# Performance work log

Hardware: AMD Instinct MI355X
Metric: run time of the kernel (lower is better)

Reference implementation:

```python
import jax, jax.numpy as jnp
import numpy as np
from jax import lax

C = 64
RED = 8
BN_EPS = 1e-5

def _conv1x1(x, W, b):
    # x: [N,C,H,W], W: [O,C] (1x1 conv kernel squeezed), b: [O]
    return jnp.einsum('nchw,oc->nohw', x, W) + b[None, :, None, None]

def _cross_attention(img, depth, Wq, bq, Wk, bk, Wv, bv, gamma):
    # img, depth: [N,C,H,W]; channel-channel attention (attn is [N,C,C])
    N, c, H, Wd = img.shape
    HW = H * Wd
    q = _conv1x1(img, Wq, bq).reshape(N, c, HW).astype(jnp.float32)
    k = _conv1x1(depth, Wk, bk).reshape(N, c, HW).astype(jnp.float32)
    v = _conv1x1(depth, Wv, bv).reshape(N, c, HW).astype(jnp.float32)
    attn = jax.nn.softmax(jnp.einsum('nci,ndi->ncd', q, k), axis=-1)  # [N,C,C]
    out = jnp.einsum('ncd,ndi->nci', attn, v).reshape(N, c, H, Wd).astype(img.dtype)
    return gamma * out + img

def _mlp(x, w1, b1, w2, b2):
    h = jax.nn.relu(x @ w1.T + b1)
    return h @ w2.T + b2

def _cbam(x, fc1_w, fc1_b, fc2_w, fc2_b, sa_w, sa_b):
    # x: [N,C,H,W]
    avg = x.mean(axis=(2, 3))          # [N,C]
    mx = x.max(axis=(2, 3))            # [N,C]
    ch = jax.nn.sigmoid(_mlp(avg, fc1_w, fc1_b, fc2_w, fc2_b)
                        + _mlp(mx, fc1_w, fc1_b, fc2_w, fc2_b))  # [N,C]
    x = x * ch[:, :, None, None]
    sp_in = jnp.stack([x.mean(axis=1), x.max(axis=1)], axis=1)   # [N,2,H,W]
    sp = lax.conv_general_dilated(sp_in, sa_w, (1, 1), 'SAME',
                                  dimension_numbers=('NCHW', 'OIHW', 'NCHW')) + sa_b[None, :, None, None]
    return x * jax.nn.sigmoid(sp)


def setup_inputs() -> dict:
    key = jax.random.key(0)
    ks = jax.random.split(key, 20)
    B, S, H, W = 2, 8, 128, 128
    s = 0.05
    d = {
        'img_feat': jax.random.normal(ks[0], (B, S, C, H, W), jnp.float32),
        'depth_feat': jax.random.normal(ks[1], (B, S, C, H, W), jnp.float32),
        # CrossAttention (shared module, used for both directions)
        'Wq': jax.random.normal(ks[2], (C, C), jnp.float32) * s,
        'bq': jax.random.normal(ks[3], (C,), jnp.float32) * s,
        'Wk': jax.random.normal(ks[4], (C, C), jnp.float32) * s,
        'bk': jax.random.normal(ks[5], (C,), jnp.float32) * s,
        'Wv': jax.random.normal(ks[6], (C, C), jnp.float32) * s,
        'bv': jax.random.normal(ks[7], (C,), jnp.float32) * s,
        'gamma': jax.random.normal(ks[8], (1,), jnp.float32) * 0.5,
        # fusion conv (3x3, 2C -> C) + BN (inference, running stats)
        'Wf': jax.random.normal(ks[9], (C, 2 * C, 3, 3), jnp.float32) * s,
        'bf': jax.random.normal(ks[10], (C,), jnp.float32) * s,
        'bn_g': jnp.ones((C,), jnp.float32),
        'bn_b': jnp.zeros((C,), jnp.float32),
        'bn_m': jax.random.normal(ks[11], (C,), jnp.float32) * s,
        'bn_v': jax.random.uniform(ks[12], (C,), jnp.float32, 0.5, 1.5),
        # CBAM channel MLP + spatial conv (7x7, 2 -> 1)
        'fc1_w': jax.random.normal(ks[13], (C // RED, C), jnp.float32) * s,
        'fc1_b': jax.random.normal(ks[14], (C // RED,), jnp.float32) * s,
        'fc2_w': jax.random.normal(ks[15], (C, C // RED), jnp.float32) * s,
        'fc2_b': jax.random.normal(ks[16], (C,), jnp.float32) * s,
        'sa_w': jax.random.normal(ks[17], (1, 2, 7, 7), jnp.float32) * s,
        'sa_b': jax.random.normal(ks[18], (1,), jnp.float32) * s,
    }
    return d


def reference(img_feat, depth_feat, Wq, bq, Wk, bk, Wv, bv, gamma,
              Wf, bf, bn_g, bn_b, bn_m, bn_v,
              fc1_w, fc1_b, fc2_w, fc2_b, sa_w, sa_b):
    B, S, c, H, W = img_feat.shape
    img = img_feat.reshape(-1, c, H, W)
    dep = depth_feat.reshape(-1, c, H, W)
    img_att = _cross_attention(img, dep, Wq, bq, Wk, bk, Wv, bv, gamma)
    dep_att = _cross_attention(dep, img, Wq, bq, Wk, bk, Wv, bv, gamma)
    fused = jnp.concatenate([img_att, dep_att], axis=1)  # [N,2C,H,W]
    fused = lax.conv_general_dilated(fused, Wf, (1, 1), 'SAME',
                                     dimension_numbers=('NCHW', 'OIHW', 'NCHW')) + bf[None, :, None, None]
    inv = bn_g * lax.rsqrt(bn_v + BN_EPS)
    fused = jax.nn.relu(fused * inv[None, :, None, None] + (bn_b - bn_m * inv)[None, :, None, None])
    fused = _cbam(fused, fc1_w, fc1_b, fc2_w, fc2_b, sa_w, sa_b)
    return fused.reshape(B, S, c, H, W)
```

## Files before the change

### kernel.cpp

```cpp
#include <hip/hip_runtime.h>
#include <math.h>


typedef __bf16 bf16_t;
typedef bf16_t bf16x8 __attribute__((ext_vector_type(8)));
typedef bf16_t bf16x4 __attribute__((ext_vector_type(4)));
typedef float  f32x4  __attribute__((ext_vector_type(4)));
typedef _Float16 f16_t;
typedef f16_t  f16x8  __attribute__((ext_vector_type(8)));

static constexpr int  CH  = 64;
static constexpr int  H   = 128;
static constexpr int  W   = 128;
static constexpr int  HW  = H * W;
static constexpr int  NI  = 16;
static constexpr int  NCK = 16;

static constexpr int W_WQ=0, W_BQ=4096, W_WK=4160, W_BK=8256, W_WV=8320, W_BV=12416,
  W_GAMMA=12480, W_WF=12481, W_BF=86209, W_BNG=86273, W_BNB=86337, W_BNM=86401,
  W_BNV=86465, W_FC1W=86529, W_FC1B=87041, W_FC2W=87049, W_FC2B=87561,
  W_SAW=87625, W_SAB=87723, W_TOTAL=87724;

static constexpr size_t OFF_GPART  = 0;
static constexpr size_t SZ_GPART   = (size_t)NI*NCK*4096*4;
static constexpr size_t OFF_SX     = OFF_GPART + SZ_GPART;
static constexpr size_t SZ_SXY     = (size_t)NI*NCK*64*4;
static constexpr size_t OFF_SY     = OFF_SX + SZ_SXY;
static constexpr size_t OFF_M1     = OFF_SY + SZ_SXY;
static constexpr size_t SZ_M       = (size_t)NI*4096*4;
static constexpr size_t OFF_M2     = OFF_M1 + SZ_M;
static constexpr size_t OFF_T1     = OFF_M2 + SZ_M;
static constexpr size_t SZ_T       = (size_t)NI*64*4;
static constexpr size_t OFF_T2     = OFF_T1 + SZ_T;
static constexpr size_t OFF_BCONST = OFF_T2 + SZ_T;
static constexpr size_t OFF_WH     = OFF_BCONST + 256;
static constexpr size_t SZ_WH      = (size_t)NI*64*9*128*2;
static constexpr size_t OFF_WINDT  = OFF_WH + SZ_WH;
static constexpr size_t SZ_WIND    = (size_t)NI*9*64*4;
static constexpr size_t OFF_IND    = OFF_WINDT + SZ_WIND;
static constexpr size_t OFF_BSUM   = OFF_IND + SZ_WIND;
static constexpr size_t SZ_BST     = (size_t)NI*64*64*4;
static constexpr size_t OFF_BMAX   = OFF_BSUM + SZ_BST;
static constexpr size_t OFF_CHS    = OFF_BMAX + SZ_BST;
static constexpr size_t OFF_SPIN   = OFF_CHS + SZ_T;
static constexpr size_t SZ_SPIN    = (size_t)NI*2*HW*4;
static constexpr size_t OFF_FLAG   = OFF_SPIN + SZ_SPIN;
static constexpr size_t OFF_WF32   = OFF_FLAG + 256;
static constexpr size_t OFF_WFT    = ((OFF_WF32 + (size_t)W_TOTAL*4 + 255) / 256) * 256;
static constexpr size_t SZ_WFT     = (size_t)9*8192*4;
static constexpr size_t OFF_P16    = ((OFF_WFT + SZ_WFT + 255) / 256) * 256;
static constexpr size_t SZ_P16     = (size_t)NI*4*HW*32*2;

__global__ __launch_bounds__(256) void k0_detect(
    const unsigned short* __restrict__ u, int* __restrict__ flag)
{
  __shared__ int bad;
  if (threadIdx.x == 0) bad = 0;
  __syncthreads();
  int local = 0;
  for (int i = threadIdx.x; i < 4096; i += 256) {
    const unsigned short v = u[2*i];
    const int e = (v >> 7) & 0xFF;
    if (e >= 0xC0) local = 1;
  }
  if (local) atomicOr(&bad, 1);
  __syncthreads();
  if (threadIdx.x == 0) flag[0] = bad;
}

struct WPack { const void* p[19]; int sz[19]; int off[19]; };

__global__ __launch_bounds__(256) void kw_convert(
    WPack wp, const int* __restrict__ flag, float* __restrict__ dst,
    float* __restrict__ WFT)
{
  const int j = blockIdx.y;
  const int i = blockIdx.x * 256 + threadIdx.x;
  if (i >= wp.sz[j]) return;
  const int f32m = flag[0];
  float v;
  if (f32m) v = ((const float*)wp.p[j])[i];
  else      v = (float)((const bf16_t*)wp.p[j])[i];
  dst[wp.off[j] + i] = v;
  if (j == 7) WFT[(i % 9) * 8192 + (i / 9)] = v;
}

__global__ __launch_bounds__(256) void kc_pack(
    const bf16_t* __restrict__ Xb, const bf16_t* __restrict__ Yb,
    const float* __restrict__ Xf, const float* __restrict__ Yf,
    const int* __restrict__ flag, f16_t* __restrict__ P16)
{
  const int lin = blockIdx.x * 256 + threadIdx.x;
  const int oct = lin & 3;
  const int p   = (lin >> 2) & 16383;
  const int s   = (lin >> 16) & 3;
  const int n   = lin >> 18;
  const int f32m = flag[0];
  const size_t nbase = (size_t)n * CH * HW;
  const int c0 = (s & 1) * 32 + oct * 8;
  const float*  Fsrc = (s < 2) ? Xf : Yf;
  const bf16_t* Bsrc = (s < 2) ? Xb : Yb;
  f16x8 h;
  #pragma unroll
  for (int j = 0; j < 8; ++j) {
    const size_t q = nbase + (size_t)(c0 + j) * HW + p;
    const float v = f32m ? Fsrc[q] : (float)Bsrc[q];
    h[j] = (f16_t)v;
  }
  *(f16x8*)(P16 + (size_t)lin * 8) = h;
}

__global__ __launch_bounds__(256) void k1_gram(
    const bf16_t* __restrict__ Xb, const bf16_t* __restrict__ Yb,
    const float* __restrict__ Xf, const float* __restrict__ Yf,
    const int* __restrict__ flag,
    float* __restrict__ Gpart, float* __restrict__ sxpart, float* __restrict__ sypart)
{
  const int chunk = blockIdx.x, n = blockIdx.y;
  const int t = threadIdx.x, lane = t & 63, wv = t >> 6;
  const int mrow = lane & 15, quad = lane >> 4;
  const int f32m = flag[0];
  const size_t nbase = (size_t)n * CH * HW;
  const int p0 = chunk * 1024 + wv * 256;

  f32x4 acc[4][4], acc2[4][4];
  #pragma unroll
  for (int i = 0; i < 4; ++i)
    #pragma unroll
    for (int j = 0; j < 4; ++j) {
      acc[i][j]  = (f32x4){0.f, 0.f, 0.f, 0.f};
      acc2[i][j] = (f32x4){0.f, 0.f, 0.f, 0.f};
    }
  float sxl[4] = {0.f,0.f,0.f,0.f}, syl[4] = {0.f,0.f,0.f,0.f};

  for (int kt = 0; kt < 8; ++kt) {
    const int pk = p0 + kt * 32 + quad * 8;
    if (f32m) {
      bf16x8 a[4], b[4], al[4], bl[4];
      #pragma unroll
      for (int mt = 0; mt < 4; ++mt) {
        const size_t ia = nbase + (size_t)(mt*16 + mrow) * HW + pk;
        float sa = 0.f, sb = 0.f;
        #pragma unroll
        for (int j = 0; j < 8; ++j) {
          const float va = Xf[ia + j];
          const bf16_t ha = (bf16_t)va;
          a[mt][j] = ha; al[mt][j] = (bf16_t)(va - (float)ha); sa += va;
          const float vb = Yf[ia + j];
          const bf16_t hb = (bf16_t)vb;
          b[mt][j] = hb; bl[mt][j] = (bf16_t)(vb - (float)hb); sb += vb;
        }
        sxl[mt] += sa; syl[mt] += sb;
      }
      #pragma unroll
      for (int mt = 0; mt < 4; ++mt)
        #pragma unroll
        for (int nt = 0; nt < 4; ++nt) {
          acc[mt][nt]  = __builtin_amdgcn_mfma_f32_16x16x32_bf16(a[mt],  b[nt],  acc[mt][nt],  0, 0, 0);
          acc2[mt][nt] = __builtin_amdgcn_mfma_f32_16x16x32_bf16(a[mt],  bl[nt], acc2[mt][nt], 0, 0, 0);
          acc2[mt][nt] = __builtin_amdgcn_mfma_f32_16x16x32_bf16(al[mt], b[nt],  acc2[mt][nt], 0, 0, 0);
        }
    } else {
      bf16x8 a[4], b[4];
      #pragma unroll
      for (int mt = 0; mt < 4; ++mt) {
        const size_t ia = nbase + (size_t)(mt*16 + mrow) * HW + pk;
        a[mt] = *(const bf16x8*)(Xb + ia);
        b[mt] = *(const bf16x8*)(Yb + ia);
        float sa = 0.f, sb = 0.f;
        #pragma unroll
        for (int j = 0; j < 8; ++j) { sa += (float)a[mt][j]; sb += (float)b[mt][j]; }
        sxl[mt] += sa; syl[mt] += sb;
      }
      #pragma unroll
      for (int mt = 0; mt < 4; ++mt)
        #pragma unroll
        for (int nt = 0; nt < 4; ++nt)
          acc[mt][nt] = __builtin_amdgcn_mfma_f32_16x16x32_bf16(a[mt], b[nt], acc[mt][nt], 0, 0, 0);
    }
  }

  #pragma unroll
  for (int mt = 0; mt < 4; ++mt) {
    sxl[mt] += __shfl_xor(sxl[mt], 16, 64); sxl[mt] += __shfl_xor(sxl[mt], 32, 64);
    syl[mt] += __shfl_xor(syl[mt], 16, 64); syl[mt] += __shfl_xor(syl[mt], 32, 64);
  }

  __shared__ float Gs[4096];
  __shared__ float sxs[64], sys[64];
  for (int w2 = 0; w2 < 4; ++w2) {
    if (wv == w2) {
      #pragma unroll
      for (int mt = 0; mt < 4; ++mt) {
        #pragma unroll
        for (int nt = 0; nt < 4; ++nt) {
          #pragma unroll
          for (int r = 0; r < 4; ++r) {
            const int c = mt*16 + quad*4 + r, d = nt*16 + mrow;
            const float val = acc[mt][nt][r] + acc2[mt][nt][r];
            if (w2 == 0) Gs[c*64 + d]  = val;
            else         Gs[c*64 + d] += val;
          }
        }
        if (quad == 0) {
          const int c = mt*16 + mrow;
          if (w2 == 0) { sxs[c] = sxl[mt];  sys[c] = syl[mt]; }
          else         { sxs[c] += sxl[mt]; sys[c] += syl[mt]; }
        }
      }
    }
    __syncthreads();
  }
  float* Gp = Gpart + ((size_t)n*NCK + chunk) * 4096;
  for (int i = t; i < 4096; i += 256) Gp[i] = Gs[i];
  if (t < 64)       sxpart[((size_t)n*NCK + chunk)*64 + t]        = sxs[t];
  else if (t < 128) sypart[((size_t)n*NCK + chunk)*64 + (t - 64)] = sys[t - 64];
}

__global__ __launch_bounds__(256, 1) void k2a_attn(
    const float* __restrict__ Gpart, const float* __restrict__ sxpart, const float* __restrict__ sypart,
    const float* __restrict__ wt,
    float* __restrict__ M1, float* __restrict__ M2,
    float* __restrict__ T1, float* __restrict__ T2)
{
  const int n = blockIdx.x, t = threadIdx.x;
  constexpr int SW = 68;
  __shared__ float Gs[4096];
  __shared__ float P1s[4096], P2s[4096];
  __shared__ float A1s[64*SW], A2s[64*SW];
  __shared__ float WQs[64*SW], WKs[64*SW], WVs[64*SW];
  __shared__ float sxs[64], sys[64], ux[64], uy[64], vx[64], vy[64];

  for (int i = t; i < 4096; i += 256) {
    const int r = i >> 6, cc = i & 63;
    WQs[r*SW + cc] = wt[W_WQ + i];
    WKs[r*SW + cc] = wt[W_WK + i];
    WVs[r*SW + cc] = wt[W_WV + i];
  }
  for (int i4 = t; i4 < 1024; i4 += 256) {
    f32x4 s = (f32x4){0.f, 0.f, 0.f, 0.f};
    for (int c2 = 0; c2 < NCK; ++c2)
      s += *(const f32x4*)(Gpart + ((size_t)n*NCK + c2)*4096 + i4*4);
    *(f32x4*)(Gs + i4*4) = s;
  }
  if (t < 64) {
    float s = 0.f; for (int c2 = 0; c2 < NCK; ++c2) s += sxpart[((size_t)n*NCK + c2)*64 + t];
    sxs[t] = s;
  } else if (t < 128) {
    const int c = t - 64;
    float s = 0.f; for (int c2 = 0; c2 < NCK; ++c2) s += sypart[((size_t)n*NCK + c2)*64 + c];
    sys[c] = s;
  }
  __syncthreads();

  {
    const int e = t & 63;
    float Greg[64], GTreg[64];
    #pragma unroll
    for (int a = 0; a < 64; ++a) Greg[a] = Gs[a*64 + e];
    #pragma unroll
    for (int a4 = 0; a4 < 16; ++a4)
      *(f32x4*)(GTreg + a4*4) = *(const f32x4*)(Gs + e*64 + a4*4);
    for (int it = 0; it < 16; ++it) {
      const int c = (t >> 6) + 4*it;
      float s1 = 0.f, s2 = 0.f;
      #pragma unroll
      for (int a4 = 0; a4 < 16; ++a4) {
        const f32x4 w4 = *(const f32x4*)(WQs + c*SW + a4*4);
        #pragma unroll
        for (int r = 0; r < 4; ++r) {
          s1 += w4[r] * Greg[a4*4 + r];
          s2 += w4[r] * GTreg[a4*4 + r];
        }
      }
      P1s[c*64 + e] = s1; P2s[c*64 + e] = s2;
    }
  }
  {
    const int which = t >> 6, c = t & 63;
    const float* Wrow = (which < 2) ? (WQs + c*SW) : (WKs + c*SW);
    const float* vecv = ((which & 1) == 0) ? sxs : sys;
    float s = 0.f;
    #pragma unroll
    for (int a = 0; a < 64; ++a) s += Wrow[a] * vecv[a];
    if      (which == 0) ux[c] = s;
    else if (which == 1) uy[c] = s;
    else if (which == 2) vx[c] = s;
    else                 vy[c] = s;
  }
  __syncthreads();

  {
    const int d = t & 63;
    float WKreg[64];
    #pragma unroll
    for (int a4 = 0; a4 < 16; ++a4)
      *(f32x4*)(WKreg + a4*4) = *(const f32x4*)(WKs + d*SW + a4*4);
    const float bkd = wt[W_BK + d];
    for (int it = 0; it < 16; ++it) {
      const int c = (t >> 6) + 4*it;
      float s1 = 0.f, s2 = 0.f;
      #pragma unroll
      for (int e4 = 0; e4 < 16; ++e4) {
        const f32x4 p1 = *(const f32x4*)(P1s + c*64 + e4*4);
        const f32x4 p2 = *(const f32x4*)(P2s + c*64 + e4*4);
        #pragma unroll
        for (int r = 0; r < 4; ++r) {
          s1 += p1[r] * WKreg[e4*4 + r];
          s2 += p2[r] * WKreg[e4*4 + r];
        }
      }
      const float bqc = wt[W_BQ + c];
      s1 += ux[c]*bkd + bqc*vy[d] + 16384.f*bqc*bkd;
      s2 += uy[c]*bkd + bqc*vx[d] + 16384.f*bqc*bkd;
      A1s[c*SW + d] = s1; A2s[c*SW + d] = s2;
    }
  }
  __syncthreads();

  if (t < 128) {
    float* R = (t < 64) ? (A1s + t*SW) : (A2s + (t - 64)*SW);
    float m = R[0];
    for (int d = 1; d < 64; ++d) m = fmaxf(m, R[d]);
    float s = 0.f;
    for (int d = 0; d < 64; ++d) { const float e2 = expf(R[d] - m); R[d] = e2; s += e2; }
    const float inv = 1.f / s;
    for (int d = 0; d < 64; ++d) R[d] *= inv;
  }
  __syncthreads();

  {
    const int e = t & 63;
    float WVreg[64];
    #pragma unroll
    for (int dd = 0; dd < 64; ++dd) WVreg[dd] = WVs[dd*SW + e];
    for (int it = 0; it < 16; ++it) {
      const int c = (t >> 6) + 4*it;
      float s1 = 0.f, s2 = 0.f;
      #pragma unroll
      for (int d4 = 0; d4 < 16; ++d4) {
        const f32x4 a1 = *(const f32x4*)(A1s + c*SW + d4*4);
        const f32x4 a2 = *(const f32x4*)(A2s + c*SW + d4*4);
        #pragma unroll
        for (int r = 0; r < 4; ++r) {
          s1 += a1[r] * WVreg[d4*4 + r];
          s2 += a2[r] * WVreg[d4*4 + r];
        }
      }
      M1[(size_t)n*4096 + c*64 + e] = s1;
      M2[(size_t)n*4096 + c*64 + e] = s2;
    }
  }
  if (t < 64) {
    float s1 = 0.f, s2 = 0.f;
    for (int d = 0; d < 64; ++d) {
      const float b = wt[W_BV + d];
      s1 += A1s[t*SW + d] * b;
      s2 += A2s[t*SW + d] * b;
    }
    T1[n*64 + t] = s1; T2[n*64 + t] = s2;
  }
}

__global__ __launch_bounds__(256) void k2b_weff(
    const float* __restrict__ wt, const float* __restrict__ WFT,
    const float* __restrict__ M1, const float* __restrict__ M2,
    const float* __restrict__ T1, const float* __restrict__ T2,
    f16_t* __restrict__ Wh, float* __restrict__ windT, float* __restrict__ bconst)
{
  const int tap = blockIdx.x, dir = blockIdx.y, n = blockIdx.z;
  const int t = threadIdx.x;
  const float g = wt[W_GAMMA];
  f16_t* Whn = Wh + (size_t)n * 64 * 9 * 128;
  const float* Mo = (dir == 0) ? (M2 + (size_t)n*4096) : (M1 + (size_t)n*4096);

  __shared__ float Wfs[8192];
  __shared__ float Ms[4096];

  for (int i4 = t; i4 < 2048; i4 += 256)
    *(f32x4*)(Wfs + i4*4) = *(const f32x4*)(WFT + (size_t)tap*8192 + i4*4);
  for (int i4 = t; i4 < 1024; i4 += 256)
    *(f32x4*)(Ms + i4*4) = *(const f32x4*)(Mo + i4*4);
  __syncthreads();

  const int e = t & 63;
  float Msreg[64];
  #pragma unroll
  for (int c = 0; c < 64; ++c) Msreg[c] = Ms[c*64 + e];
  const int coff = dir ? 0 : 64;
  const int boff = dir ? 64 : 0;
  for (int it = 0; it < 16; ++it) {
    const int o = (t >> 6) + 4*it;
    const float inv = wt[W_BNG + o] * rsqrtf(wt[W_BNV + o] + 1e-5f);
    const float base = Wfs[o*128 + boff + e];
    float s = 0.f;
    #pragma unroll
    for (int c4 = 0; c4 < 16; ++c4) {
      const f32x4 w4 = *(const f32x4*)(Wfs + o*128 + coff + c4*4);
      #pragma unroll
      for (int r = 0; r < 4; ++r) s += w4[r] * Msreg[c4*4 + r];
    }
    Whn[(o*9 + tap)*128 + dir*64 + e] = (f16_t)(inv * (base + g * s));
  }

  if (dir == 0 && t < 64) {
    const int o = t;
    const float inv = wt[W_BNG + o] * rsqrtf(wt[W_BNV + o] + 1e-5f);
    float s = 0.f;
    for (int c = 0; c < 64; ++c)
      s += wt[W_WF + (o*128 + c)*9 + tap]      * T1[n*64 + c]
         + wt[W_WF + (o*128 + 64 + c)*9 + tap] * T2[n*64 + c];
    windT[((size_t)n*9 + tap)*64 + o] = inv * g * s;
    if (tap == 0 && n == 0)
      bconst[o] = wt[W_BF + o]*inv + wt[W_BNB + o] - wt[W_BNM + o]*inv;
  }
}

__global__ __launch_bounds__(512) void k3_conv(
    const bf16_t* __restrict__ Xb, const bf16_t* __restrict__ Yb,
    const float* __restrict__ Xf, const float* __restrict__ Yf,
    const int* __restrict__ flag,
    const f16_t* __restrict__ Wh, const float* __restrict__ bconst,
    const float* __restrict__ windT,
    const f16_t* __restrict__ P16, const int useP16,
    bf16_t* __restrict__ fusedB, float* __restrict__ fusedF,
    float* __restrict__ bsum, float* __restrict__ bmax)
{
  __shared__ __attribute__((aligned(16))) f16_t sbuf[6][130][40];
  __shared__ float sind[576], sconst[64];
  __shared__ float ssum[8][64], smax[8][64];
  const int rp = blockIdx.x, n = blockIdx.y;
  const int t = threadIdx.x, lane = t & 63, wv = t >> 6;
  const int l15 = lane & 15, quad = lane >> 4;
  const int ly = wv >> 1, ch2 = wv & 1;
  const int f32m = flag[0];
  const size_t nbase = (size_t)n * CH * HW;
  const f16_t* __restrict__ Whn = Wh + (size_t)n * 64 * 9 * 128;

  for (int i = t; i < 576; i += 512) {
    const int g = i >> 6, o = i & 63;
    const int yc = g / 3, xc = g % 3;
    const int ky0 = (yc == 0) ? 1 : 0, ky1 = (yc == 2) ? 1 : 2;
    const int kx0 = (xc == 0) ? 1 : 0, kx1 = (xc == 2) ? 1 : 2;
    float sv = 0.f;
    for (int ky = ky0; ky <= ky1; ++ky)
      for (int kx = kx0; kx <= kx1; ++kx)
        sv += windT[((size_t)n*9 + ky*3 + kx)*64 + o];
    sind[i] = sv;
  }
  if (t < 64) sconst[t] = bconst[t];
  if (t < 384) {
    const int r = t >> 6, cs = (t >> 5) & 1, sl = t & 31;
    sbuf[r][cs ? 129 : 0][sl] = (f16_t)0.f;
  }

  f32x4 acc[4][4];
  #pragma unroll
  for (int i = 0; i < 4; ++i)
    #pragma unroll
    for (int j = 0; j < 4; ++j) acc[i][j] = (f32x4){0.f, 0.f, 0.f, 0.f};

  if (useP16) {
    const int oct = t & 3;
    const int x   = t >> 2;
    const f16_t* __restrict__ PnB = P16 + (size_t)(n*4) * HW * 32;
    f16x8 h[6];

    #define K3_STAGE_LOAD(S)                                                  \
      { const f16_t* __restrict__ Pn = PnB + (size_t)(S) * HW * 32;           \
        _Pragma("unroll")                                                     \
        for (int i = 0; i < 6; ++i) {                                         \
          const int gy = rp*4 - 1 + i;                                        \
          f16x8 v;                                                            \
          _Pragma("unroll")                                                   \
          for (int k2 = 0; k2 < 8; ++k2) v[k2] = (f16_t)0.f;                  \
          if (gy >= 0 && gy < H)                                              \
            v = *(const f16x8*)(Pn + ((size_t)(gy*128 + x) * 32 + oct*8));    \
          h[i] = v;                                                           \
        } }
    #define K3_STAGE_WRITE()                                                  \
      { const int colL = x + 1;                                               \
        _Pragma("unroll")                                                     \
        for (int i = 0; i < 6; ++i)                                           \
          *(f16x8*)&sbuf[i][colL][(oct ^ (colL & 3)) * 8] = h[i];             \
      }

    K3_STAGE_LOAD(0)
    K3_STAGE_WRITE()
    for (int s = 0; s < 4; ++s) {
      if (s < 3) K3_STAGE_LOAD(s + 1)
      asm volatile("s_waitcnt lgkmcnt(0)" ::: "memory");
      __builtin_amdgcn_s_barrier();
      __builtin_amdgcn_s_setprio(1);
      #pragma unroll
      for (int tap = 0; tap < 9; ++tap) {
        const int ky = tap / 3, kx = tap % 3;
        f16x8 bfr[4];
        #pragma unroll
        for (int nt = 0; nt < 4; ++nt) {
          const int o = nt*16 + l15;
          bfr[nt] = *(const f16x8*)(Whn + ((o*9 + tap)*128 + s*32 + quad*8));
        }
        f16x8 afr[4];
        const int row = ly + ky;
        #pragma unroll
        for (int mt = 0; mt < 4; ++mt) {
          const int col = ch2*64 + mt*16 + l15 + kx;
          afr[mt] = *(const f16x8*)&sbuf[row][col][(quad ^ (col & 3)) * 8];
        }
        #pragma unroll
        for (int mt = 0; mt < 4; ++mt)
          #pragma unroll
          for (int nt = 0; nt < 4; ++nt)
            acc[mt][nt] = __builtin_amdgcn_mfma_f32_16x16x32_f16(afr[mt], bfr[nt], acc[mt][nt], 0, 0, 0);
      }
      __builtin_amdgcn_s_setprio(0);
      __builtin_amdgcn_s_barrier();
      if (s < 3) K3_STAGE_WRITE()
    }
    #undef K3_STAGE_LOAD
    #undef K3_STAGE_WRITE
  } else {
    const int cstage = t & 127, rsel = t >> 7;
    for (int s = 0; s < 4; ++s) {
      __syncthreads();
      #pragma unroll
      for (int pass = 0; pass < 2; ++pass) {
        const int r = rsel + 4*pass;
        if (r < 6) {
          const int gy = rp*4 - 1 + r;
          const bool valid = (gy >= 0) && (gy < H);
          const int colL = cstage + 1;
          #pragma unroll
          for (int oct = 0; oct < 4; ++oct) {
            f16x8 hh;
            #pragma unroll
            for (int j = 0; j < 8; ++j) {
              const int g = s*32 + oct*8 + j;
              float v = 0.f;
              if (valid) {
                const size_t q = nbase + (size_t)(g & 63)*HW + gy*W + cstage;
                v = (g < 64) ? (f32m ? Xf[q] : (float)Xb[q])
                             : (f32m ? Yf[q] : (float)Yb[q]);
              }
              hh[j] = (f16_t)v;
            }
            *(f16x8*)&sbuf[r][colL][(oct ^ (colL & 3)) * 8] = hh;
          }
        }
      }
      __syncthreads();
      #pragma unroll
      for (int tap = 0; tap < 9; ++tap) {
        const int ky = tap / 3, kx = tap % 3;
        f16x8 bfr[4];
        #pragma unroll
        for (int nt = 0; nt < 4; ++nt) {
          const int o = nt*16 + l15;
          bfr[nt] = *(const f16x8*)(Whn + ((o*9 + tap)*128 + s*32 + quad*8));
        }
        f16x8 afr[4];
        const int row = ly + ky;
        #pragma unroll
        for (int mt = 0; mt < 4; ++mt) {
          const int col = ch2*64 + mt*16 + l15 + kx;
          afr[mt] = *(const f16x8*)&sbuf[row][col][(quad ^ (col & 3)) * 8];
        }
        #pragma unroll
        for (int mt = 0; mt < 4; ++mt)
          #pragma unroll
          for (int nt = 0; nt < 4; ++nt)
            acc[mt][nt] = __builtin_amdgcn_mfma_f32_16x16x32_f16(afr[mt], bfr[nt], acc[mt][nt], 0, 0, 0);
      }
    }
  }

  const int y = rp*4 + ly;
  const int yc = (y == 0) ? 0 : (y == H-1) ? 2 : 1;
  #pragma unroll
  for (int nt = 0; nt < 4; ++nt) {
    const int o = nt*16 + l15;
    const float bc = sconst[o];
    float ssm = 0.f, smx = 0.f;
    #pragma unroll
    for (int mt = 0; mt < 4; ++mt) {
      const int xb = ch2*64 + mt*16 + quad*4;
      f32x4 vals;
      #pragma unroll
      for (int r = 0; r < 4; ++r) {
        const int x = xb + r;
        const int xc = (x == 0) ? 0 : (x == W-1) ? 2 : 1;
        float v = acc[mt][nt][r] + bc + sind[(yc*3 + xc)*64 + o];
        v = fmaxf(v, 0.f);
        vals[r] = v; ssm += v; smx = fmaxf(smx, v);
      }
      const size_t off = nbase + (size_t)o*HW + y*W + xb;
      if (f32m) {
        *(f32x4*)(fusedF + off) = vals;
      } else {
        bf16x4 pv;
        #pragma unroll
        for (int r = 0; r < 4; ++r) pv[r] = (bf16_t)vals[r];
        *(bf16x4*)(fusedB + off) = pv;
      }
    }
    ssm += __shfl_xor(ssm, 16, 64); ssm += __shfl_xor(ssm, 32, 64);
    smx = fmaxf(smx, __shfl_xor(smx, 16, 64));
    smx = fmaxf(smx, __shfl_xor(smx, 32, 64));
    if (quad == 0) { ssum[wv][o] = ssm; smax[wv][o] = smx; }
  }
  __syncthreads();
  if (t < 64) {
    float S = 0.f, M = 0.f;
    #pragma unroll
    for (int w2 = 0; w2 < 8; ++w2) {
      S += ssum[w2][t];
      M = fmaxf(M, smax[w2][t]);
    }
    bsum[((size_t)n*32 + rp)*64 + t] = S;
    bmax[((size_t)n*32 + rp)*64 + t] = M;
  }
}

__global__ __launch_bounds__(64) void k4_chgate(
    const float* __restrict__ bsum, const float* __restrict__ bmax,
    const float* __restrict__ wt, float* __restrict__ chout)
{
  const int n = blockIdx.x, t = threadIdx.x;
  __shared__ float avg[64], mxs[64], h1[8], h2[8];
  float S = 0.f, M = 0.f;
  for (int rp = 0; rp < 32; ++rp) {
    S += bsum[((size_t)n*32 + rp)*64 + t];
    M = fmaxf(M, bmax[((size_t)n*32 + rp)*64 + t]);
  }
  avg[t] = S * (1.f / 16384.f);
  mxs[t] = M;
  __syncthreads();
  if (t < 8) {
    float s = wt[W_FC1B + t];
    for (int c = 0; c < 64; ++c) s += wt[W_FC1W + t*64 + c] * avg[c];
    h1[t] = fmaxf(s, 0.f);
  } else if (t < 16) {
    const int r = t - 8;
    float s = wt[W_FC1B + r];
    for (int c = 0; c < 64; ++c) s += wt[W_FC1W + r*64 + c] * mxs[c];
    h2[r] = fmaxf(s, 0.f);
  }
  __syncthreads();
  float s = 2.f * wt[W_FC2B + t];
  for (int r = 0; r < 8; ++r) s += wt[W_FC2W + t*8 + r] * (h1[r] + h2[r]);
  chout[n*64 + t] = 1.f / (1.f + expf(-s));
}

__global__ __launch_bounds__(128) void k5_spin(
    const bf16_t* __restrict__ fusedB, const float* __restrict__ fusedF,
    const int* __restrict__ flag,
    const float* __restrict__ chs, float* __restrict__ spin)
{
  const int n = blockIdx.y;
  const int p0 = (blockIdx.x * 128 + threadIdx.x) * 8;
  const int f32m = flag[0];
  const size_t nbase = (size_t)n * CH * HW;
  const float* c = chs + n * 64;
  float s[8], m[8];
  #pragma unroll
  for (int k = 0; k < 8; ++k) { s[k] = 0.f; m[k] = 0.f; }
  if (f32m) {
    for (int o = 0; o < 64; ++o) {
      const float co = c[o];
      const float* q = fusedF + nbase + (size_t)o*HW + p0;
      const f32x4 a = *(const f32x4*)q;
      const f32x4 b = *(const f32x4*)(q + 4);
      #pragma unroll
      for (int k = 0; k < 4; ++k) {
        const float v0 = a[k] * co; s[k]   += v0; m[k]   = fmaxf(m[k],   v0);
        const float v1 = b[k] * co; s[4+k] += v1; m[4+k] = fmaxf(m[4+k], v1);
      }
    }
  } else {
    for (int o = 0; o < 64; ++o) {
      const float co = c[o];
      const bf16x8 a = *(const bf16x8*)(fusedB + nbase + (size_t)o*HW + p0);
      #pragma unroll
      for (int k = 0; k < 8; ++k) {
        const float v = (float)a[k] * co; s[k] += v; m[k] = fmaxf(m[k], v);
      }
    }
  }
  f32x4 o0, o1, o2, o3;
  #pragma unroll
  for (int k = 0; k < 4; ++k) {
    o0[k] = s[k]   * (1.f / 64.f);
    o1[k] = s[4+k] * (1.f / 64.f);
    o2[k] = m[k];
    o3[k] = m[4+k];
  }
  *(f32x4*)(spin + (size_t)n*2*HW + p0)          = o0;
  *(f32x4*)(spin + (size_t)n*2*HW + p0 + 4)      = o1;
  *(f32x4*)(spin + (size_t)n*2*HW + HW + p0)     = o2;
  *(f32x4*)(spin + (size_t)n*2*HW + HW + p0 + 4) = o3;
}

__global__ __launch_bounds__(128) void k6_final(
    bf16_t* __restrict__ fusedB, float* __restrict__ fusedF,
    const int* __restrict__ flag,
    const float* __restrict__ chs, const float* __restrict__ spin,
    const float* __restrict__ wt)
{
  const int n = blockIdx.y;
  const int p0 = (blockIdx.x * 128 + threadIdx.x) * 8;
  const int y = p0 >> 7, x0 = p0 & 127;
  const int f32m = flag[0];
  const float* s0 = spin + (size_t)n*2*HW;
  const float* s1 = s0 + HW;
  float acc[8];
  {
    const float sab = wt[W_SAB];
    #pragma unroll
    for (int k = 0; k < 8; ++k) acc[k] = sab;
  }
  for (int j = 0; j < 7; ++j) {
    const int yy = y + j - 3;
    if (yy < 0 || yy >= H) continue;
    const float* r0 = s0 + yy*W;
    const float* r1 = s1 + yy*W;
    float v0[14], v1[14];
    #pragma unroll
    for (int ii = 0; ii < 14; ++ii) {
      const int xx = x0 + ii - 3;
      const bool ok = (xx >= 0) && (xx < W);
      v0[ii] = ok ? r0[xx] : 0.f;
      v1[ii] = ok ? r1[xx] : 0.f;
    }
    #pragma unroll
    for (int i = 0; i < 7; ++i) {
      const float w0 = wt[W_SAW + j*7 + i];
      const float w1 = wt[W_SAW + 49 + j*7 + i];
      #pragma unroll
      for (int k = 0; k < 8; ++k)
        acc[k] += w0 * v0[i+k] + w1 * v1[i+k];
    }
  }
  float sp[8];
  #pragma unroll
  for (int k = 0; k < 8; ++k) sp[k] = 1.f / (1.f + expf(-acc[k]));
  const size_t nbase = (size_t)n * CH * HW;
  const float* c = chs + n * 64;
  if (f32m) {
    for (int o = 0; o < 64; ++o) {
      const float co = c[o];
      float* q = fusedF + nbase + (size_t)o*HW + p0;
      f32x4 a = *(f32x4*)q;
      f32x4 b = *(f32x4*)(q + 4);
      #pragma unroll
      for (int k = 0; k < 4; ++k) {
        a[k] = a[k] * co * sp[k];
        b[k] = b[k] * co * sp[4+k];
      }
      *(f32x4*)q       = a;
      *(f32x4*)(q + 4) = b;
    }
  } else {
    for (int o = 0; o < 64; ++o) {
      const float co = c[o];
      bf16_t* q = fusedB + nbase + (size_t)o*HW + p0;
      bf16x8 a = *(bf16x8*)q;
      #pragma unroll
      for (int k = 0; k < 8; ++k)
        a[k] = (bf16_t)((float)a[k] * co * sp[k]);
      *(bf16x8*)q = a;
    }
  }
}

extern "C" void kernel_launch(void* const* d_in, const int* in_sizes, int n_in,
                              void* d_out, int out_size, void* d_ws, size_t ws_size,
                              hipStream_t stream)
{
  (void)n_in; (void)out_size; (void)in_sizes;
  char* ws = (char*)d_ws;
  float*  Gpart  = (float*)(ws + OFF_GPART);
  float*  sxp    = (float*)(ws + OFF_SX);
  float*  syp    = (float*)(ws + OFF_SY);
  float*  M1     = (float*)(ws + OFF_M1);
  float*  M2     = (float*)(ws + OFF_M2);
  float*  T1     = (float*)(ws + OFF_T1);
  float*  T2     = (float*)(ws + OFF_T2);
  float*  bconst = (float*)(ws + OFF_BCONST);
  f16_t*  Wh     = (f16_t*)(ws + OFF_WH);
  float*  windT  = (float*)(ws + OFF_WINDT);
  float*  bsum   = (float*)(ws + OFF_BSUM);
  float*  bmax   = (float*)(ws + OFF_BMAX);
  float*  chs    = (float*)(ws + OFF_CHS);
  float*  spin   = (float*)(ws + OFF_SPIN);
  int*    flag   = (int*)  (ws + OFF_FLAG);
  float*  wf32   = (float*)(ws + OFF_WF32);
  float*  wft    = (float*)(ws + OFF_WFT);
  f16_t*  P16    = (f16_t*)(ws + OFF_P16);
  bf16_t* fusedB = (bf16_t*)d_out;
  float*  fusedF = (float*)d_out;

  const int useP16 = (ws_size >= OFF_P16 + SZ_P16) ? 1 : 0;

  const bf16_t* imgB = (const bf16_t*)d_in[0];
  const bf16_t* depB = (const bf16_t*)d_in[1];
  const float*  imgF = (const float*) d_in[0];
  const float*  depF = (const float*) d_in[1];

  WPack wp;
  static const int wsz[19] = {4096,64,4096,64,4096,64,1,73728,64,64,64,64,64,512,8,512,64,98,1};
  static const int woff[19] = {W_WQ,W_BQ,W_WK,W_BK,W_WV,W_BV,W_GAMMA,W_WF,W_BF,W_BNG,
                               W_BNB,W_BNM,W_BNV,W_FC1W,W_FC1B,W_FC2W,W_FC2B,W_SAW,W_SAB};
  for (int j = 0; j < 19; ++j) { wp.p[j] = d_in[2 + j]; wp.sz[j] = wsz[j]; wp.off[j] = woff[j]; }

  hipLaunchKernelGGL(k0_detect, dim3(1), dim3(256), 0, stream,
                     (const unsigned short*)d_in[0], flag);
  hipLaunchKernelGGL(kw_convert, dim3(288, 19), dim3(256), 0, stream, wp, flag, wf32, wft);
  if (useP16)
    hipLaunchKernelGGL(kc_pack, dim3(16384), dim3(256), 0, stream,
                       imgB, depB, imgF, depF, flag, P16);
  hipLaunchKernelGGL(k1_gram,  dim3(NCK, NI), dim3(256), 0, stream,
                     imgB, depB, imgF, depF, flag, Gpart, sxp, syp);
  hipLaunchKernelGGL(k2a_attn, dim3(NI), dim3(256), 0, stream,
                     Gpart, sxp, syp, wf32, M1, M2, T1, T2);
  hipLaunchKernelGGL(k2b_weff, dim3(9, 2, NI), dim3(256), 0, stream,
                     wf32, wft, M1, M2, T1, T2, Wh, windT, bconst);
  hipLaunchKernelGGL(k3_conv,  dim3(32, NI), dim3(512), 0, stream,
                     imgB, depB, imgF, depF, flag, Wh, bconst, windT,
                     P16, useP16, fusedB, fusedF, bsum, bmax);
  hipLaunchKernelGGL(k4_chgate, dim3(NI), dim3(64), 0, stream,
                     bsum, bmax, wf32, chs);
  hipLaunchKernelGGL(k5_spin,  dim3(16, NI), dim3(128), 0, stream,
                     fusedB, fusedF, flag, chs, spin);
  hipLaunchKernelGGL(k6_final, dim3(16, NI), dim3(128), 0, stream,
                     fusedB, fusedF, flag, chs, spin, wf32);
}
```

Measured before the change: 453.6 us.

## Merge weight/pack kernels, split attention per direction and channel half, widen gate

Fuses the weight-conversion and fp16 packing kernels into one launch, removing a kernel boundary. Splits the attention kernel into 4 blocks per sample, one per direction and half of the output channels, so 64 blocks run instead of 16. Each block still rebuilds the full Gram sum in shared memory, which adds redundant global reads. The channel-gate kernel now uses 256 threads to split its 32-partial reduction four ways. Together these aim to cut launch overhead and raise parallelism in the small serial stages.

Result: faster. 423.5 us (-6.7%).

```diff
diff --git a/kernel.cpp b/kernel.cpp
--- a/kernel.cpp
+++ b/kernel.cpp
@@ -70,44 +70,46 @@
 
 struct WPack { const void* p[19]; int sz[19]; int off[19]; };
 
-__global__ __launch_bounds__(256) void kw_convert(
+__global__ __launch_bounds__(256) void kwc_prep(
     WPack wp, const int* __restrict__ flag, float* __restrict__ dst,
-    float* __restrict__ WFT)
-{
-  const int j = blockIdx.y;
-  const int i = blockIdx.x * 256 + threadIdx.x;
-  if (i >= wp.sz[j]) return;
-  const int f32m = flag[0];
-  float v;
-  if (f32m) v = ((const float*)wp.p[j])[i];
-  else      v = (float)((const bf16_t*)wp.p[j])[i];
-  dst[wp.off[j] + i] = v;
-  if (j == 7) WFT[(i % 9) * 8192 + (i / 9)] = v;
-}
-
-__global__ __launch_bounds__(256) void kc_pack(
+    float* __restrict__ WFT,
     const bf16_t* __restrict__ Xb, const bf16_t* __restrict__ Yb,
     const float* __restrict__ Xf, const float* __restrict__ Yf,
-    const int* __restrict__ flag, f16_t* __restrict__ P16)
-{
-  const int lin = blockIdx.x * 256 + threadIdx.x;
-  const int oct = lin & 3;
-  const int p   = (lin >> 2) & 16383;
-  const int s   = (lin >> 16) & 3;
-  const int n   = lin >> 18;
+    f16_t* __restrict__ P16, const int useP16)
+{
+  const int b = blockIdx.x;
   const int f32m = flag[0];
-  const size_t nbase = (size_t)n * CH * HW;
-  const int c0 = (s & 1) * 32 + oct * 8;
-  const float*  Fsrc = (s < 2) ? Xf : Yf;
-  const bf16_t* Bsrc = (s < 2) ? Xb : Yb;
-  f16x8 h;
-  #pragma unroll
-  for (int j = 0; j < 8; ++j) {
-    const size_t q = nbase + (size_t)(c0 + j) * HW + p;
-    const float v = f32m ? Fsrc[q] : (float)Bsrc[q];
-    h[j] = (f16_t)v;
-  }
-  *(f16x8*)(P16 + (size_t)lin * 8) = h;
+  if (b < 16384) {
+    if (!useP16) return;
+    const int lin = b * 256 + threadIdx.x;
+    const int oct = lin & 3;
+    const int p   = (lin >> 2) & 16383;
+    const int s   = (lin >> 16) & 3;
+    const int n   = lin >> 18;
+    const size_t nbase = (size_t)n * CH * HW;
+    const int c0 = (s & 1) * 32 + oct * 8;
+    const float*  Fsrc = (s < 2) ? Xf : Yf;
+    const bf16_t* Bsrc = (s < 2) ? Xb : Yb;
+    f16x8 h;
+    #pragma unroll
+    for (int j = 0; j < 8; ++j) {
+      const size_t q = nbase + (size_t)(c0 + j) * HW + p;
+      const float v = f32m ? Fsrc[q] : (float)Bsrc[q];
+      h[j] = (f16_t)v;
+    }
+    *(f16x8*)(P16 + (size_t)lin * 8) = h;
+  } else {
+    const int bb = b - 16384;
+    const int j  = bb / 288;
+    const int bx = bb % 288;
+    const int i = bx * 256 + threadIdx.x;
+    if (i >= wp.sz[j]) return;
+    float v;
+    if (f32m) v = ((const float*)wp.p[j])[i];
+    else      v = (float)((const bf16_t*)wp.p[j])[i];
+    dst[wp.off[j] + i] = v;
+    if (j == 7) WFT[(i % 9) * 8192 + (i / 9)] = v;
+  }
 }
 
 __global__ __launch_bounds__(256) void k1_gram(
@@ -223,13 +225,16 @@
     float* __restrict__ M1, float* __restrict__ M2,
     float* __restrict__ T1, float* __restrict__ T2)
 {
-  const int n = blockIdx.x, t = threadIdx.x;
+  const int bx = blockIdx.x, n = blockIdx.y;
+  const int dir  = bx & 1;
+  const int c0   = (bx >> 1) * 32;
+  const int t = threadIdx.x;
   constexpr int SW = 68;
   __shared__ float Gs[4096];
-  __shared__ float P1s[4096], P2s[4096];
-  __shared__ float A1s[64*SW], A2s[64*SW];
+  __shared__ float Ps[4096];
+  __shared__ float As[64*SW];
   __shared__ float WQs[64*SW], WKs[64*SW], WVs[64*SW];
-  __shared__ float sxs[64], sys[64], ux[64], uy[64], vx[64], vy[64];
+  __shared__ float sxs[64], sys[64], uu[64], vv[64];
 
   for (int i = t; i < 4096; i += 256) {
     const int r = i >> 6, cc = i & 63;
@@ -255,38 +260,42 @@
 
   {
     const int e = t & 63;
-    float Greg[64], GTreg[64];
-    #pragma unroll
-    for (int a = 0; a < 64; ++a) Greg[a] = Gs[a*64 + e];
-    #pragma unroll
-    for (int a4 = 0; a4 < 16; ++a4)
-      *(f32x4*)(GTreg + a4*4) = *(const f32x4*)(Gs + e*64 + a4*4);
-    for (int it = 0; it < 16; ++it) {
-      const int c = (t >> 6) + 4*it;
-      float s1 = 0.f, s2 = 0.f;
+    float Greg[64];
+    if (dir == 0) {
+      #pragma unroll
+      for (int a = 0; a < 64; ++a) Greg[a] = Gs[a*64 + e];
+    } else {
+      #pragma unroll
+      for (int a4 = 0; a4 < 16; ++a4)
+        *(f32x4*)(Greg + a4*4) = *(const f32x4*)(Gs + e*64 + a4*4);
+    }
+    for (int it = 0; it < 8; ++it) {
+      const int c = c0 + (t >> 6) + 4*it;
+      float s1 = 0.f;
       #pragma unroll
       for (int a4 = 0; a4 < 16; ++a4) {
         const f32x4 w4 = *(const f32x4*)(WQs + c*SW + a4*4);
         #pragma unroll
-        for (int r = 0; r < 4; ++r) {
-          s1 += w4[r] * Greg[a4*4 + r];
-          s2 += w4[r] * GTreg[a4*4 + r];
-        }
-      }
-      P1s[c*64 + e] = s1; P2s[c*64 + e] = s2;
+        for (int r = 0; r < 4; ++r) s1 += w4[r] * Greg[a4*4 + r];
+      }
+      Ps[c*64 + e] = s1;
     }
   }
   {
-    const int which = t >> 6, c = t & 63;
-    const float* Wrow = (which < 2) ? (WQs + c*SW) : (WKs + c*SW);
-    const float* vecv = ((which & 1) == 0) ? sxs : sys;
-    float s = 0.f;
-    #pragma unroll
-    for (int a = 0; a < 64; ++a) s += Wrow[a] * vecv[a];
-    if      (which == 0) ux[c] = s;
-    else if (which == 1) uy[c] = s;
-    else if (which == 2) vx[c] = s;
-    else                 vy[c] = s;
+    const int c = t & 63;
+    if (t < 64) {
+      const float* vecv = dir ? sys : sxs;
+      float s = 0.f;
+      #pragma unroll
+      for (int a = 0; a < 64; ++a) s += WQs[c*SW + a] * vecv[a];
+      uu[c] = s;
+    } else if (t < 128) {
+      const float* vecv = dir ? sxs : sys;
+      float s = 0.f;
+      #pragma unroll
+      for (int a = 0; a < 64; ++a) s += WKs[c*SW + a] * vecv[a];
+      vv[c] = s;
+    }
   }
   __syncthreads();
 
@@ -297,29 +306,24 @@
     for (int a4 = 0; a4 < 16; ++a4)
       *(f32x4*)(WKreg + a4*4) = *(const f32x4*)(WKs + d*SW + a4*4);
     const float bkd = wt[W_BK + d];
-    for (int it = 0; it < 16; ++it) {
-      const int c = (t >> 6) + 4*it;
-      float s1 = 0.f, s2 = 0.f;
+    for (int it = 0; it < 8; ++it) {
+      const int c = c0 + (t >> 6) + 4*it;
+      float s1 = 0.f;
       #pragma unroll
       for (int e4 = 0; e4 < 16; ++e4) {
-        const f32x4 p1 = *(const f32x4*)(P1s + c*64 + e4*4);
-        const f32x4 p2 = *(const f32x4*)(P2s + c*64 + e4*4);
-        #pragma unroll
-        for (int r = 0; r < 4; ++r) {
-          s1 += p1[r] * WKreg[e4*4 + r];
-          s2 += p2[r] * WKreg[e4*4 + r];
-        }
+        const f32x4 p1 = *(const f32x4*)(Ps + c*64 + e4*4);
+        #pragma unroll
+        for (int r = 0; r < 4; ++r) s1 += p1[r] * WKreg[e4*4 + r];
       }
       const float bqc = wt[W_BQ + c];
-      s1 += ux[c]*bkd + bqc*vy[d] + 16384.f*bqc*bkd;
-      s2 += uy[c]*bkd + bqc*vx[d] + 16384.f*bqc*bkd;
-      A1s[c*SW + d] = s1; A2s[c*SW + d] = s2;
-    }
-  }
-  __syncthreads();
-
-  if (t < 128) {
-    float* R = (t < 64) ? (A1s + t*SW) : (A2s + (t - 64)*SW);
+      s1 += uu[c]*bkd + bqc*vv[d] + 16384.f*bqc*bkd;
+      As[c*SW + d] = s1;
+    }
+  }
+  __syncthreads();
+
+  if (t < 32) {
+    float* R = As + (c0 + t)*SW;
     float m = R[0];
     for (int d = 1; d < 64; ++d) m = fmaxf(m, R[d]);
     float s = 0.f;
@@ -334,31 +338,24 @@
     float WVreg[64];
     #pragma unroll
     for (int dd = 0; dd < 64; ++dd) WVreg[dd] = WVs[dd*SW + e];
-    for (int it = 0; it < 16; ++it) {
-      const int c = (t >> 6) + 4*it;
-      float s1 = 0.f, s2 = 0.f;
+    float* Mo = (dir ? M2 : M1) + (size_t)n*4096;
+    for (int it = 0; it < 8; ++it) {
+      const int c = c0 + (t >> 6) + 4*it;
+      float s1 = 0.f;
       #pragma unroll
       for (int d4 = 0; d4 < 16; ++d4) {
-        const f32x4 a1 = *(const f32x4*)(A1s + c*SW + d4*4);
-        const f32x4 a2 = *(const f32x4*)(A2s + c*SW + d4*4);
-        #pragma unroll
-        for (int r = 0; r < 4; ++r) {
-          s1 += a1[r] * WVreg[d4*4 + r];
-          s2 += a2[r] * WVreg[d4*4 + r];
-        }
-      }
-      M1[(size_t)n*4096 + c*64 + e] = s1;
-      M2[(size_t)n*4096 + c*64 + e] = s2;
-    }
-  }
-  if (t < 64) {
-    float s1 = 0.f, s2 = 0.f;
-    for (int d = 0; d < 64; ++d) {
-      const float b = wt[W_BV + d];
-      s1 += A1s[t*SW + d] * b;
-      s2 += A2s[t*SW + d] * b;
-    }
-    T1[n*64 + t] = s1; T2[n*64 + t] = s2;
+        const f32x4 a1 = *(const f32x4*)(As + c*SW + d4*4);
+        #pragma unroll
+        for (int r = 0; r < 4; ++r) s1 += a1[r] * WVreg[d4*4 + r];
+      }
+      Mo[c*64 + e] = s1;
+    }
+  }
+  if (t < 32) {
+    const int c = c0 + t;
+    float s1 = 0.f;
+    for (int d = 0; d < 64; ++d) s1 += As[c*SW + d] * wt[W_BV + d];
+    (dir ? T2 : T1)[n*64 + c] = s1;
   }
 }
 
@@ -622,19 +619,27 @@
   }
 }
 
-__global__ __launch_bounds__(64) void k4_chgate(
+__global__ __launch_bounds__(256) void k4_chgate(
     const float* __restrict__ bsum, const float* __restrict__ bmax,
     const float* __restrict__ wt, float* __restrict__ chout)
 {
   const int n = blockIdx.x, t = threadIdx.x;
+  const int o = t & 63, part = t >> 6;
+  __shared__ float ps[4][64], pm[4][64];
   __shared__ float avg[64], mxs[64], h1[8], h2[8];
   float S = 0.f, M = 0.f;
-  for (int rp = 0; rp < 32; ++rp) {
-    S += bsum[((size_t)n*32 + rp)*64 + t];
-    M = fmaxf(M, bmax[((size_t)n*32 + rp)*64 + t]);
-  }
-  avg[t] = S * (1.f / 16384.f);
-  mxs[t] = M;
+  for (int rp = part*8; rp < part*8 + 8; ++rp) {
+    S += bsum[((size_t)n*32 + rp)*64 + o];
+    M = fmaxf(M, bmax[((size_t)n*32 + rp)*64 + o]);
+  }
+  ps[part][o] = S; pm[part][o] = M;
+  __syncthreads();
+  if (t < 64) {
+    const float Sa = ((ps[0][t] + ps[1][t]) + ps[2][t]) + ps[3][t];
+    const float Ma = fmaxf(fmaxf(pm[0][t], pm[1][t]), fmaxf(pm[2][t], pm[3][t]));
+    avg[t] = Sa * (1.f / 16384.f);
+    mxs[t] = Ma;
+  }
   __syncthreads();
   if (t < 8) {
     float s = wt[W_FC1B + t];
@@ -647,9 +652,11 @@
     h2[r] = fmaxf(s, 0.f);
   }
   __syncthreads();
-  float s = 2.f * wt[W_FC2B + t];
-  for (int r = 0; r < 8; ++r) s += wt[W_FC2W + t*8 + r] * (h1[r] + h2[r]);
-  chout[n*64 + t] = 1.f / (1.f + expf(-s));
+  if (t < 64) {
+    float s = 2.f * wt[W_FC2B + t];
+    for (int r = 0; r < 8; ++r) s += wt[W_FC2W + t*8 + r] * (h1[r] + h2[r]);
+    chout[n*64 + t] = 1.f / (1.f + expf(-s));
+  }
 }
 
 __global__ __launch_bounds__(128) void k5_spin(
@@ -815,20 +822,18 @@
 
   hipLaunchKernelGGL(k0_detect, dim3(1), dim3(256), 0, stream,
                      (const unsigned short*)d_in[0], flag);
-  hipLaunchKernelGGL(kw_convert, dim3(288, 19), dim3(256), 0, stream, wp, flag, wf32, wft);
-  if (useP16)
-    hipLaunchKernelGGL(kc_pack, dim3(16384), dim3(256), 0, stream,
-                       imgB, depB, imgF, depF, flag, P16);
+  hipLaunchKernelGGL(kwc_prep, dim3(16384 + 5472), dim3(256), 0, stream,
+                     wp, flag, wf32, wft, imgB, depB, imgF, depF, P16, useP16);
   hipLaunchKernelGGL(k1_gram,  dim3(NCK, NI), dim3(256), 0, stream,
                      imgB, depB, imgF, depF, flag, Gpart, sxp, syp);
-  hipLaunchKernelGGL(k2a_attn, dim3(NI), dim3(256), 0, stream,
+  hipLaunchKernelGGL(k2a_attn, dim3(4, NI), dim3(256), 0, stream,
                      Gpart, sxp, syp, wf32, M1, M2, T1, T2);
   hipLaunchKernelGGL(k2b_weff, dim3(9, 2, NI), dim3(256), 0, stream,
                      wf32, wft, M1, M2, T1, T2, Wh, windT, bconst);
   hipLaunchKernelGGL(k3_conv,  dim3(32, NI), dim3(512), 0, stream,
                      imgB, depB, imgF, depF, flag, Wh, bconst, windT,
                      P16, useP16, fusedB, fusedF, bsum, bmax);
-  hipLaunchKernelGGL(k4_chgate, dim3(NI), dim3(64), 0, stream,
+  hipLaunchKernelGGL(k4_chgate, dim3(NI), dim3(256), 0, stream,
                      bsum, bmax, wf32, chs);
   hipLaunchKernelGGL(k5_spin,  dim3(16, NI), dim3(128), 0, stream,
                      fusedB, fusedF, flag, chs, spin);
```
